# Kernel optimization log

Measured on AMD Instinct MI355X. Metric: run time of the kernel, lower is better.

The kernel has to match this reference:

```python
import jax, jax.numpy as jnp
import numpy as np

D_MODEL = 1024
N_HEADS = 16
HEAD_DIM = D_MODEL // N_HEADS
B, L = 2, 2048


def setup_inputs() -> dict:
    key = jax.random.key(0)
    ks = jax.random.split(key, 9)
    s = 1.0 / np.sqrt(D_MODEL)
    return {
        "hidden_states": jax.random.normal(ks[0], (B, L, D_MODEL), dtype=jnp.float32),
        "Wq": jax.random.uniform(ks[1], (D_MODEL, D_MODEL), jnp.float32, -s, s),
        "bq": jax.random.uniform(ks[2], (D_MODEL,), jnp.float32, -s, s),
        "Wk": jax.random.uniform(ks[3], (D_MODEL, D_MODEL), jnp.float32, -s, s),
        "bk": jax.random.uniform(ks[4], (D_MODEL,), jnp.float32, -s, s),
        "Wv": jax.random.uniform(ks[5], (D_MODEL, D_MODEL), jnp.float32, -s, s),
        "bv": jax.random.uniform(ks[6], (D_MODEL,), jnp.float32, -s, s),
        "Wo": jax.random.uniform(ks[7], (D_MODEL, D_MODEL), jnp.float32, -s, s),
        "bo": jax.random.uniform(ks[8], (D_MODEL,), jnp.float32, -s, s),
    }


def reference(hidden_states, Wq, bq, Wk, bk, Wv, bv, Wo, bo):
    b, l, d = hidden_states.shape
    h, hd = N_HEADS, HEAD_DIM
    scale = jnp.sqrt(jnp.asarray(hd, hidden_states.dtype))
    # projections (weights stored as [in, out], equivalent to torch Linear W.T)
    Q = (hidden_states @ Wq + bq).reshape(b, l, h, hd).transpose(0, 2, 1, 3)
    K = (hidden_states @ Wk + bk).reshape(b, l, h, hd).transpose(0, 2, 1, 3)
    V = (hidden_states @ Wv + bv).reshape(b, l, h, hd).transpose(0, 2, 1, 3)
    # [b, h, l, l] scores with causal mask
    scores = jnp.einsum("bhqd,bhkd->bhqk", Q, K) / scale
    causal = jnp.tril(jnp.ones((l, l), dtype=bool))
    scores = jnp.where(causal, scores, jnp.asarray(-jnp.inf, scores.dtype))
    weights = jax.nn.softmax(scores, axis=-1)
    out = jnp.einsum("bhqk,bhkd->bhqd", weights, V)
    out = out.transpose(0, 2, 1, 3).reshape(b, l, d)
    return out @ Wo + bo
```

## Files before the change

### kernel.cpp

```cpp
#include <hip/hip_runtime.h>

typedef unsigned short u16;
typedef unsigned int u32;
typedef __attribute__((ext_vector_type(8))) short bf16x8;
typedef __attribute__((ext_vector_type(4))) float f32x4;

__device__ __forceinline__ u16 f2bf(float f) {
    union { float f; u32 u; } x; x.f = f;
    u32 r = x.u + 0x7FFFu + ((x.u >> 16) & 1u);
    return (u16)(r >> 16);
}

__device__ __forceinline__ u16 f2bf_fast(float f) {
    union { float f; u32 u; } x; x.f = f;
    return (u16)((x.u + 0x8000u) >> 16);
}

__device__ __forceinline__ void gload16(const u16* g, u16* l) {
    __builtin_amdgcn_global_load_lds(
        (const __attribute__((address_space(1))) void*)g,
        (__attribute__((address_space(3))) void*)l,
        16, 0, 0);
}

__device__ __forceinline__ f32x4 mfma16(bf16x8 a, bf16x8 b, f32x4 c) {
    return __builtin_amdgcn_mfma_f32_16x16x32_bf16(a, b, c, 0, 0, 0);
}


__global__ __launch_bounds__(256) void cvt_x(const float* __restrict__ in, u16* __restrict__ out, int n4) {
    int i = blockIdx.x * blockDim.x + threadIdx.x;
    if (i >= n4) return;
    float4 v = ((const float4*)in)[i];
    u16* o = out + (size_t)i * 4;
    o[0] = f2bf(v.x); o[1] = f2bf(v.y); o[2] = f2bf(v.z); o[3] = f2bf(v.w);
}

__global__ __launch_bounds__(256) void transpose_w4(const float* __restrict__ Wq, const float* __restrict__ Wk,
                                                    const float* __restrict__ Wv, const float* __restrict__ Wo,
                                                    const float* __restrict__ bq, const float* __restrict__ bk,
                                                    const float* __restrict__ bv,
                                                    u16* __restrict__ qkvt, u16* __restrict__ wot,
                                                    float* __restrict__ bqkv) {
    __shared__ float tile[32][33];
    const float* in;
    u16* out;
    if (blockIdx.z == 0)      { in = Wq; out = qkvt; }
    else if (blockIdx.z == 1) { in = Wk; out = qkvt + 1024 * 1024; }
    else if (blockIdx.z == 2) { in = Wv; out = qkvt + 2 * 1024 * 1024; }
    else                      { in = Wo; out = wot; }
    if (blockIdx.z == 3 && blockIdx.x == 0 && blockIdx.y == 0) {
        for (int i = threadIdx.x; i < 3072; i += 256)
            bqkv[i] = (i < 1024) ? bq[i] : ((i < 2048) ? bk[i - 1024] : bv[i - 2048]);
    }
    const int bx = blockIdx.x * 32, by = blockIdx.y * 32;
    const int tx = threadIdx.x & 31, ty4 = (threadIdx.x >> 5) * 4;
#pragma unroll
    for (int j = 0; j < 4; ++j)
        tile[ty4 + j][tx] = in[(size_t)(by + ty4 + j) * 1024 + bx + tx];
    __syncthreads();
#pragma unroll
    for (int j = 0; j < 4; ++j)
        out[(size_t)(bx + ty4 + j) * 1024 + by + tx] = f2bf(tile[tx][ty4 + j]);
}

template<int MODE>
__global__ __launch_bounds__(256) void gemm128(const u16* __restrict__ A, const u16* __restrict__ Bt,
                                               const float* __restrict__ bias,
                                               u16* __restrict__ oq, u16* __restrict__ ok, u16* __restrict__ ov,
                                               float* __restrict__ of, int K)
{
    __shared__ u16 As[128 * 64];
    __shared__ u16 Bs[128 * 64];

    const int n0 = blockIdx.x * 128;
    const int m0 = blockIdx.y * 128;
    const int t = threadIdx.x;
    const int w = t >> 6, lane = t & 63;
    const int g = lane >> 4, lr = lane & 15;
    const int wm = w >> 1, wn = w & 1;
    const int sw = lr & 7;

    const int srow = lane >> 3;
    const int schunk = (lane & 7) ^ srow;
    const u16* pA = A  + (size_t)(m0 + w * 8 + srow) * K + schunk * 8;
    const u16* pB = Bt + (size_t)(n0 + w * 8 + srow) * K + schunk * 8;
    u16* lA = &As[w * 512 + lane * 8];
    u16* lB = &Bs[w * 512 + lane * 8];

    const int sa_row = (wm * 64 + lr) * 64;
    const int sb_row = (wn * 64 + lr) * 64;

    f32x4 acc[4][4] = {};

    for (int k0 = 0; k0 < K; k0 += 64) {
        __syncthreads();
#pragma unroll
        for (int i = 0; i < 4; ++i) {
            gload16(pA + (size_t)i * 32 * K + k0, lA + i * 2048);
            gload16(pB + (size_t)i * 32 * K + k0, lB + i * 2048);
        }
        __syncthreads();
#pragma unroll
        for (int kk = 0; kk < 2; ++kk) {
            const int cofs = ((kk * 4 + g) ^ sw) * 8;
            bf16x8 af[4], bf[4];
#pragma unroll
            for (int mi = 0; mi < 4; ++mi) af[mi] = *(const bf16x8*)&As[sa_row + mi * 16 * 64 + cofs];
#pragma unroll
            for (int ni = 0; ni < 4; ++ni) bf[ni] = *(const bf16x8*)&Bs[sb_row + ni * 16 * 64 + cofs];
#pragma unroll
            for (int mi = 0; mi < 4; ++mi)
#pragma unroll
                for (int ni = 0; ni < 4; ++ni)
                    acc[mi][ni] = mfma16(af[mi], bf[ni], acc[mi][ni]);
        }
    }

#pragma unroll
    for (int mi = 0; mi < 4; ++mi) {
#pragma unroll
        for (int ni = 0; ni < 4; ++ni) {
            const int col = n0 + wn * 64 + ni * 16 + lr;
            const int row0 = m0 + wm * 64 + mi * 16 + g * 4;
            const float bs = bias[col];
            if (MODE == 0) {
                const int mat = col >> 10;
                const int nn = col & 1023;
                const int h = nn >> 6, d = nn & 63;
                const int b = row0 >> 11, ll0 = row0 & 2047;
                const int bh = b * 16 + h;
                if (mat == 0) {
#pragma unroll
                    for (int j = 0; j < 4; ++j)
                        oq[((size_t)bh * 2048 + ll0 + j) * 64 + d] =
                            f2bf((acc[mi][ni][j] + bs) * 0.1803368801111244f);
                } else if (mat == 1) {
#pragma unroll
                    for (int j = 0; j < 4; ++j)
                        ok[((size_t)bh * 2048 + ll0 + j) * 64 + d] = f2bf(acc[mi][ni][j] + bs);
                } else {
                    union { ushort4 s4; u16 u[4]; } pk;
#pragma unroll
                    for (int j = 0; j < 4; ++j) pk.u[j] = f2bf(acc[mi][ni][j] + bs);
                    *(ushort4*)&ov[((size_t)bh * 64 + d) * 2048 + ll0] = pk.s4;
                }
            } else {
#pragma unroll
                for (int j = 0; j < 4; ++j)
                    of[(size_t)(row0 + j) * 1024 + col] = acc[mi][ni][j] + bs;
            }
        }
    }
}

__global__ __launch_bounds__(256) void attn(const u16* __restrict__ Q, const u16* __restrict__ Kg,
                                            const u16* __restrict__ Vt, u16* __restrict__ O,
                                            float* __restrict__ Opart, float* __restrict__ Mp,
                                            float* __restrict__ Lp, int do_split)
{
    __shared__ u16 Ks[64 * 64];
    __shared__ u16 Vs[64 * 64];
    __shared__ u16 Ps[4][16 * 64];

    const int bh = blockIdx.x;
    int qb, k_lo, k_hi, split;
    if (!do_split) {
        qb = 31 - (int)blockIdx.y; k_lo = 0; k_hi = qb + 1; split = -1;
    } else {
        const int y = (int)blockIdx.y;
        if (y < 32) {
            qb = 16 + (y >> 1);
            split = y & 1;
            const int mid = (qb + 1) >> 1;
            k_lo = split ? mid : 0;
            k_hi = split ? qb + 1 : mid;
        } else {
            qb = 47 - y; k_lo = 0; k_hi = qb + 1; split = -1;
        }
    }
    const int q0 = qb * 64;
    const int t = threadIdx.x;
    const int w = t >> 6, lane = t & 63;
    const int g = lane >> 4, lr = lane & 15;
    const int qw = q0 + w * 16;
    const int sw = lr & 7;

    const u16* Qb = Q  + (size_t)bh * 2048 * 64;
    const u16* Kb = Kg + (size_t)bh * 2048 * 64;
    const u16* Vb = Vt + (size_t)bh * 64 * 2048;

    const bf16x8 qf0 = *(const bf16x8*)&Qb[(size_t)(qw + lr) * 64 + g * 8];
    const bf16x8 qf1 = *(const bf16x8*)&Qb[(size_t)(qw + lr) * 64 + 32 + g * 8];

    const short one = (short)0x3F80;
    const bf16x8 vones = {one, one, one, one, one, one, one, one};

    f32x4 oacc[4] = {};
    f32x4 lsacc = {};
    float mrun = -1e30f;

    int bpaddr[4];
#pragma unroll
    for (int j = 0; j < 4; ++j) bpaddr[j] = (20 * g + j) * 4;

    const int pw_base = lr * 64;
    const int g2h = g >> 1;
    const int wic2 = (2 * g) & 3;

    bf16x8 kreg[2], vreg[2];
    const int srow0 = t >> 3, sch = t & 7;
    auto issue = [&](int kb) {
#pragma unroll
        for (int i = 0; i < 2; ++i) {
            const int row = srow0 + i * 32;
            kreg[i] = *(const bf16x8*)&Kb[(size_t)(kb * 64 + row) * 64 + sch * 8];
            vreg[i] = *(const bf16x8*)&Vb[(size_t)row * 2048 + kb * 64 + sch * 8];
        }
    };
    auto commit = [&]() {
#pragma unroll
        for (int i = 0; i < 2; ++i) {
            const int row = srow0 + i * 32;
            const int chs = sch ^ (row & 7);
            *(bf16x8*)&Ks[row * 64 + chs * 8] = kreg[i];
            *(bf16x8*)&Vs[row * 64 + chs * 8] = vreg[i];
        }
    };

    issue(k_lo);

    for (int kb = k_lo; kb < k_hi; ++kb) {
        const int k0 = kb * 64;
        __syncthreads();
        commit();
        __syncthreads();
        if (kb + 1 < k_hi) issue(kb + 1);

        f32x4 s[4] = {};
        __builtin_amdgcn_s_setprio(1);
#pragma unroll
        for (int ni = 0; ni < 4; ++ni) {
            const int row = ni * 16 + lr;
            bf16x8 kf0 = *(const bf16x8*)&Ks[row * 64 + (g ^ sw) * 8];
            bf16x8 kf1 = *(const bf16x8*)&Ks[row * 64 + ((4 + g) ^ sw) * 8];
            s[ni] = mfma16(kf0, qf0, s[ni]);
            s[ni] = mfma16(kf1, qf1, s[ni]);
        }
        __builtin_amdgcn_s_setprio(0);

        if (kb == qb) {
            const int qq = qw + lr;
#pragma unroll
            for (int ni = 0; ni < 4; ++ni)
#pragma unroll
                for (int j = 0; j < 4; ++j)
                    if (k0 + ni * 16 + g * 4 + j > qq) s[ni][j] = -1e30f;
        }

        float pm = fmaxf(fmaxf(fmaxf(s[0][0], s[0][1]), fmaxf(s[0][2], s[0][3])),
                         fmaxf(fmaxf(s[1][0], s[1][1]), fmaxf(s[1][2], s[1][3])));
        pm = fmaxf(pm, fmaxf(fmaxf(fmaxf(s[2][0], s[2][1]), fmaxf(s[2][2], s[2][3])),
                             fmaxf(fmaxf(s[3][0], s[3][1]), fmaxf(s[3][2], s[3][3]))));
        pm = fmaxf(pm, __shfl_xor(pm, 16));
        pm = fmaxf(pm, __shfl_xor(pm, 32));

        if (__any(pm > mrun + 8.f)) {
            const float mn = fmaxf(mrun, pm);
            const float r = __builtin_amdgcn_exp2f(mrun - mn);
            mrun = mn;
            const int ri = __float_as_int(r);
#pragma unroll
            for (int j = 0; j < 4; ++j) {
                const float ro = __int_as_float(__builtin_amdgcn_ds_bpermute(bpaddr[j], ri));
                lsacc[j] *= ro;
#pragma unroll
                for (int df = 0; df < 4; ++df) oacc[df][j] *= ro;
            }
        }

#pragma unroll
        for (int ni = 0; ni < 4; ++ni) {
            const int c8 = 2 * ni + g2h;
#pragma unroll
            for (int jp = 0; jp < 2; ++jp) {
                const float plo = __builtin_amdgcn_exp2f(s[ni][2 * jp]     - mrun);
                const float phi = __builtin_amdgcn_exp2f(s[ni][2 * jp + 1] - mrun);
                const u32 pr = (u32)f2bf_fast(plo) | ((u32)f2bf_fast(phi) << 16);
                const int wic = wic2 + jp;
                *(u32*)&Ps[w][pw_base + (c8 ^ sw) * 8 + wic * 2] = pr;
            }
        }

        const bf16x8 p0 = *(const bf16x8*)&Ps[w][lr * 64 + (g ^ sw) * 8];
        const bf16x8 p1 = *(const bf16x8*)&Ps[w][lr * 64 + ((4 + g) ^ sw) * 8];
        __builtin_amdgcn_s_setprio(1);
        lsacc = mfma16(p0, vones, lsacc);
        lsacc = mfma16(p1, vones, lsacc);
#pragma unroll
        for (int df = 0; df < 4; ++df) {
            const int row = df * 16 + lr;
            bf16x8 vf0 = *(const bf16x8*)&Vs[row * 64 + (g ^ sw) * 8];
            bf16x8 vf1 = *(const bf16x8*)&Vs[row * 64 + ((4 + g) ^ sw) * 8];
            oacc[df] = mfma16(p0, vf0, oacc[df]);
            oacc[df] = mfma16(p1, vf1, oacc[df]);
        }
        __builtin_amdgcn_s_setprio(0);
    }

    if (split < 0) {
        const int b = bh >> 4, h = bh & 15;
#pragma unroll
        for (int j = 0; j < 4; ++j) {
            const float inv = 1.f / lsacc[j];
            const int l = qw + g * 4 + j;
#pragma unroll
            for (int df = 0; df < 4; ++df)
                O[((size_t)b * 2048 + l) * 1024 + h * 64 + df * 16 + lr] = f2bf(oacc[df][j] * inv);
        }
    } else {
        float* Ob = Opart + ((size_t)split * 32 + bh) * (1024 * 64);
        const int rb = qw - 1024 + 4 * g;
#pragma unroll
        for (int j = 0; j < 4; ++j)
#pragma unroll
            for (int df = 0; df < 4; ++df)
                Ob[(size_t)(rb + j) * 64 + df * 16 + lr] = oacc[df][j];
        if (lr == 0) {
#pragma unroll
            for (int j = 0; j < 4; ++j)
                Lp[(split * 32 + bh) * 1024 + rb + j] = lsacc[j];
        }
        if (g == 0)
            Mp[(split * 32 + bh) * 1024 + (qw - 1024) + lr] = mrun;
    }
}

__global__ __launch_bounds__(256) void attn_merge(const float* __restrict__ Opart,
                                                  const float* __restrict__ Mp,
                                                  const float* __restrict__ Lp,
                                                  u16* __restrict__ O)
{
    const int idx = blockIdx.x * 256 + threadIdx.x;
    const int d  = idx & 63;
    const int rr = (idx >> 6) & 1023;
    const int bh = idx >> 16;
    const int si = bh * 1024 + rr;
    const float m0 = Mp[si], m1 = Mp[32 * 1024 + si];
    const float l0 = Lp[si], l1 = Lp[32 * 1024 + si];
    const float M  = fmaxf(m0, m1);
    const float w0 = __builtin_amdgcn_exp2f(m0 - M);
    const float w1 = __builtin_amdgcn_exp2f(m1 - M);
    const float o0 = Opart[(size_t)si * 64 + d];
    const float o1 = Opart[(size_t)(32 * 1024 + si) * 64 + d];
    const float o  = (w0 * o0 + w1 * o1) / (w0 * l0 + w1 * l1);
    const int b = bh >> 4, h = bh & 15;
    const int r = 1024 + rr;
    O[((size_t)b * 2048 + r) * 1024 + h * 64 + d] = f2bf(o);
}


extern "C" void kernel_launch(void* const* d_in, const int* in_sizes, int n_in,
                              void* d_out, int out_size, void* d_ws, size_t ws_size,
                              hipStream_t stream)
{
    const float* hs = (const float*)d_in[0];
    const float* Wq = (const float*)d_in[1];
    const float* bq = (const float*)d_in[2];
    const float* Wk = (const float*)d_in[3];
    const float* bk = (const float*)d_in[4];
    const float* Wv = (const float*)d_in[5];
    const float* bv = (const float*)d_in[6];
    const float* Wo = (const float*)d_in[7];
    const float* bo = (const float*)d_in[8];
    float* out = (float*)d_out;

    char* ws = (char*)d_ws;
    u16*   Xbf   = (u16*)(ws);
    u16*   Wqkvt = (u16*)(ws + (8ull  << 20));
    u16*   Wot   = (u16*)(ws + (14ull << 20));
    float* bqkv  = (float*)(ws + (16ull << 20));
    u16*   Qbuf  = (u16*)(ws + (17ull << 20));
    u16*   Kbuf  = (u16*)(ws + (25ull << 20));
    u16*   Vtbuf = (u16*)(ws + (33ull << 20));
    u16*   Abuf  = Xbf;
    float* Opart = (float*)(ws + (42ull << 20));
    float* Mpart = (float*)(ws + (58ull << 20));
    float* Lpart = (float*)(ws + (58ull << 20) + (512ull << 10));

    const int do_split = (ws_size >= (59ull << 20)) ? 1 : 0;

    cvt_x<<<4096, 256, 0, stream>>>(hs, Xbf, 4096 * 1024 / 4);
    transpose_w4<<<dim3(32, 32, 4), 256, 0, stream>>>(Wq, Wk, Wv, Wo, bq, bk, bv, Wqkvt, Wot, bqkv);

    gemm128<0><<<dim3(24, 32), 256, 0, stream>>>(Xbf, Wqkvt, bqkv, Qbuf, Kbuf, Vtbuf, nullptr, 1024);

    if (do_split) {
        attn<<<dim3(32, 48), 256, 0, stream>>>(Qbuf, Kbuf, Vtbuf, Abuf, Opart, Mpart, Lpart, 1);
        attn_merge<<<8192, 256, 0, stream>>>(Opart, Mpart, Lpart, Abuf);
    } else {
        attn<<<dim3(32, 32), 256, 0, stream>>>(Qbuf, Kbuf, Vtbuf, Abuf, nullptr, nullptr, nullptr, 0);
    }

    gemm128<1><<<dim3(8, 32), 256, 0, stream>>>(Abuf, Wot, bo, nullptr, nullptr, nullptr, out, 1024);
}
```

Baseline: 125.7 us.

## Use 256x256 double-buffered tile GEMM for QKV projection

```diff
diff --git a/kernel.cpp b/kernel.cpp
--- a/kernel.cpp
+++ b/kernel.cpp
@@ -64,15 +64,120 @@
         out[(size_t)(bx + ty4 + j) * 1024 + by + tx] = f2bf(tile[tx][ty4 + j]);
 }
 
-template<int MODE>
-__global__ __launch_bounds__(256) void gemm128(const u16* __restrict__ A, const u16* __restrict__ Bt,
-                                               const float* __restrict__ bias,
-                                               u16* __restrict__ oq, u16* __restrict__ ok, u16* __restrict__ ov,
-                                               float* __restrict__ of, int K)
+__global__ __launch_bounds__(512, 2) void gemm256_qkv(const u16* __restrict__ A, const u16* __restrict__ Bt,
+                                                      const float* __restrict__ bias,
+                                                      u16* __restrict__ oq, u16* __restrict__ ok,
+                                                      u16* __restrict__ ov)
+{
+    __shared__ u16 As[2][256 * 64];
+    __shared__ u16 Bs[2][256 * 64];
+
+    const int n0 = blockIdx.x * 256;
+    const int m0 = blockIdx.y * 256;
+    const int t = threadIdx.x;
+    const int lane = t & 63;
+    const int w = t >> 6;
+    const int g = lane >> 4, lr = lane & 15;
+    const int wm = w >> 2, wn = w & 3;
+    const int sw = lr & 7;
+
+    const int srow8 = t >> 3;
+    const int sch = t & 7;
+    const int schunk = sch ^ (srow8 & 7);
+    const u16* pA = A  + (size_t)(m0 + srow8) * 1024 + schunk * 8;
+    const u16* pB = Bt + (size_t)(n0 + srow8) * 1024 + schunk * 8;
+    const int ldst = srow8 * 64 + sch * 8;
+
+    const int arow_base = (wm * 128 + lr) * 64;
+    const int brow_base = (wn * 64 + lr) * 64;
+
+    f32x4 acc[8][4] = {};
+
+#pragma unroll
+    for (int i = 0; i < 4; ++i) {
+        gload16(pA + (size_t)(i * 64) * 1024, &As[0][i * 4096 + ldst]);
+        gload16(pB + (size_t)(i * 64) * 1024, &Bs[0][i * 4096 + ldst]);
+    }
+    asm volatile("s_waitcnt vmcnt(0)" ::: "memory");
+    __builtin_amdgcn_s_barrier();
+
+    for (int kt = 0; kt < 16; ++kt) {
+        const int cur = kt & 1, nxt = cur ^ 1;
+        const int kcol = (kt + 1) * 64;
+        const bool pf = (kt < 15);
+#pragma unroll
+        for (int q = 0; q < 4; ++q) {
+            const int qm = q >> 1, qn = q & 1;
+            if (pf) {
+                gload16(pA + (size_t)(q * 64) * 1024 + kcol, &As[nxt][q * 4096 + ldst]);
+                gload16(pB + (size_t)(q * 64) * 1024 + kcol, &Bs[nxt][q * 4096 + ldst]);
+            }
+            __builtin_amdgcn_s_setprio(1);
+#pragma unroll
+            for (int kk = 0; kk < 2; ++kk) {
+                const int cofs = ((kk * 4 + g) ^ sw) * 8;
+                bf16x8 af[4], bf[2];
+#pragma unroll
+                for (int mi = 0; mi < 4; ++mi)
+                    af[mi] = *(const bf16x8*)&As[cur][arow_base + (qm * 64 + mi * 16) * 64 + cofs];
+#pragma unroll
+                for (int ni = 0; ni < 2; ++ni)
+                    bf[ni] = *(const bf16x8*)&Bs[cur][brow_base + (qn * 32 + ni * 16) * 64 + cofs];
+#pragma unroll
+                for (int mi = 0; mi < 4; ++mi)
+#pragma unroll
+                    for (int ni = 0; ni < 2; ++ni)
+                        acc[qm * 4 + mi][qn * 2 + ni] =
+                            mfma16(af[mi], bf[ni], acc[qm * 4 + mi][qn * 2 + ni]);
+            }
+            __builtin_amdgcn_s_setprio(0);
+            if (q < 3) {
+                __builtin_amdgcn_s_barrier();
+            } else {
+                asm volatile("s_waitcnt vmcnt(0)" ::: "memory");
+                __builtin_amdgcn_s_barrier();
+            }
+        }
+    }
+
+#pragma unroll
+    for (int mi = 0; mi < 8; ++mi) {
+#pragma unroll
+        for (int ni = 0; ni < 4; ++ni) {
+            const int col = n0 + wn * 64 + ni * 16 + lr;
+            const int row0 = m0 + wm * 128 + mi * 16 + g * 4;
+            const float bs = bias[col];
+            const int mat = col >> 10;
+            const int nn = col & 1023;
+            const int h = nn >> 6, d = nn & 63;
+            const int b = row0 >> 11, ll0 = row0 & 2047;
+            const int bh = b * 16 + h;
+            if (mat == 0) {
+#pragma unroll
+                for (int j = 0; j < 4; ++j)
+                    oq[((size_t)bh * 2048 + ll0 + j) * 64 + d] =
+                        f2bf((acc[mi][ni][j] + bs) * 0.1803368801111244f);
+            } else if (mat == 1) {
+#pragma unroll
+                for (int j = 0; j < 4; ++j)
+                    ok[((size_t)bh * 2048 + ll0 + j) * 64 + d] = f2bf(acc[mi][ni][j] + bs);
+            } else {
+                union { ushort4 s4; u16 u[4]; } pk;
+#pragma unroll
+                for (int j = 0; j < 4; ++j) pk.u[j] = f2bf(acc[mi][ni][j] + bs);
+                *(ushort4*)&ov[((size_t)bh * 64 + d) * 2048 + ll0] = pk.s4;
+            }
+        }
+    }
+}
+
+__global__ __launch_bounds__(256) void gemm128_o(const u16* __restrict__ A, const u16* __restrict__ Bt,
+                                                 const float* __restrict__ bias, float* __restrict__ of)
 {
     __shared__ u16 As[128 * 64];
     __shared__ u16 Bs[128 * 64];
 
+    const int K = 1024;
     const int n0 = blockIdx.x * 128;
     const int m0 = blockIdx.y * 128;
     const int t = threadIdx.x;
@@ -124,32 +229,9 @@
             const int col = n0 + wn * 64 + ni * 16 + lr;
             const int row0 = m0 + wm * 64 + mi * 16 + g * 4;
             const float bs = bias[col];
-            if (MODE == 0) {
-                const int mat = col >> 10;
-                const int nn = col & 1023;
-                const int h = nn >> 6, d = nn & 63;
-                const int b = row0 >> 11, ll0 = row0 & 2047;
-                const int bh = b * 16 + h;
-                if (mat == 0) {
-#pragma unroll
-                    for (int j = 0; j < 4; ++j)
-                        oq[((size_t)bh * 2048 + ll0 + j) * 64 + d] =
-                            f2bf((acc[mi][ni][j] + bs) * 0.1803368801111244f);
-                } else if (mat == 1) {
-#pragma unroll
-                    for (int j = 0; j < 4; ++j)
-                        ok[((size_t)bh * 2048 + ll0 + j) * 64 + d] = f2bf(acc[mi][ni][j] + bs);
-                } else {
-                    union { ushort4 s4; u16 u[4]; } pk;
-#pragma unroll
-                    for (int j = 0; j < 4; ++j) pk.u[j] = f2bf(acc[mi][ni][j] + bs);
-                    *(ushort4*)&ov[((size_t)bh * 64 + d) * 2048 + ll0] = pk.s4;
-                }
-            } else {
-#pragma unroll
-                for (int j = 0; j < 4; ++j)
-                    of[(size_t)(row0 + j) * 1024 + col] = acc[mi][ni][j] + bs;
-            }
+#pragma unroll
+            for (int j = 0; j < 4; ++j)
+                of[(size_t)(row0 + j) * 1024 + col] = acc[mi][ni][j] + bs;
         }
     }
 }
@@ -393,7 +475,7 @@
     cvt_x<<<4096, 256, 0, stream>>>(hs, Xbf, 4096 * 1024 / 4);
     transpose_w4<<<dim3(32, 32, 4), 256, 0, stream>>>(Wq, Wk, Wv, Wo, bq, bk, bv, Wqkvt, Wot, bqkv);
 
-    gemm128<0><<<dim3(24, 32), 256, 0, stream>>>(Xbf, Wqkvt, bqkv, Qbuf, Kbuf, Vtbuf, nullptr, 1024);
+    gemm256_qkv<<<dim3(12, 16), 512, 0, stream>>>(Xbf, Wqkvt, bqkv, Qbuf, Kbuf, Vtbuf);
 
     if (do_split) {
         attn<<<dim3(32, 48), 256, 0, stream>>>(Qbuf, Kbuf, Vtbuf, Abuf, Opart, Mpart, Lpart, 1);
@@ -402,5 +484,5 @@
         attn<<<dim3(32, 32), 256, 0, stream>>>(Qbuf, Kbuf, Vtbuf, Abuf, nullptr, nullptr, nullptr, 0);
     }
 
-    gemm128<1><<<dim3(8, 32), 256, 0, stream>>>(Abuf, Wot, bo, nullptr, nullptr, nullptr, out, 1024);
-}
+    gemm128_o<<<dim3(8, 32), 256, 0, stream>>>(Abuf, Wot, bo, out);
+}
```

Measured after the change: 140.2 us. 1.12x slower.
